# Optimization experiments

Hardware: AMD Instinct MI355X
Metric: run time of the kernel (lower is better)

The kernel has to match this reference:

```python
import jax, jax.numpy as jnp
import numpy as np
import math

N = 65536
IN_FEATURES = 64
OUT_FEATURES = 64
N_MODES = 32
N_BASIS = 1 + 2 * N_MODES


def setup_inputs() -> dict:
    key = jax.random.key(0)
    k1, k2 = jax.random.split(key)
    x = jax.random.normal(k1, (N, IN_FEATURES), dtype=jnp.float32)
    coeffs = jax.random.normal(k2, (OUT_FEATURES, IN_FEATURES, N_BASIS), dtype=jnp.float32) * 0.1
    bias = jnp.zeros((OUT_FEATURES,), dtype=jnp.float32)
    return {"x": x, "coeffs": coeffs, "bias": bias}


def reference(x, coeffs, bias):
    # freqs: [modes] = (1..modes) * pi
    freqs = jnp.arange(1, N_MODES + 1, dtype=x.dtype) * jnp.asarray(math.pi, dtype=x.dtype)
    x_flat = x.reshape(-1, IN_FEATURES)                      # [n, i]
    angles = x_flat[..., None] * freqs                       # [n, i, m]
    ones = jnp.ones(x_flat.shape + (1,), dtype=x.dtype)      # [n, i, 1]
    basis = jnp.concatenate([ones, jnp.sin(angles), jnp.cos(angles)], axis=-1)  # [n, i, b]
    out = jnp.einsum('oib,nib->no', coeffs, basis) + bias    # [n, o]
    return out.reshape(*x.shape[:-1], OUT_FEATURES)
```

## Files before the change

### kernel.cpp

```cpp
#include <hip/hip_runtime.h>
#include <hip/hip_bf16.h>


typedef __bf16 bf16x8 __attribute__((ext_vector_type(8)));
typedef float  f32x4  __attribute__((ext_vector_type(4)));
typedef float  f32x16 __attribute__((ext_vector_type(16)));

#define PI_F 3.14159265358979323846f

__global__ __launch_bounds__(256) void fkan_repack(
    const float* __restrict__ coeffs, __bf16* __restrict__ Bp,
    float* __restrict__ bias2sum) {
  int gid = blockIdx.x * 256 + threadIdx.x;
  if (gid >= 64 * 64 * 65) return;
  float v = coeffs[gid];
  int b  = gid % 65;
  int oi = gid / 65;
  int i = oi & 63;
  int o = oi >> 6;
  if (b == 0) {
    atomicAdd(&bias2sum[o], v);
    return;
  }
  int m  = (b - 1) & 31;
  int sc = (b >= 33) ? 1 : 0;
  int kc = i >> 3;
  int kq = (i >> 2) & 1;
  int cc = o >> 5;
  int frag = (m * 8 + kc) * 2 + cc;
  int lane = kq * 32 + (o & 31);
  int t = 2 * (i & 3) + sc;
  Bp[frag * 512 + lane * 8 + t] = (__bf16)v;
}

__device__ __forceinline__ void stage_slice(const __bf16* __restrict__ Bp,
                                            __bf16* dst, int m, int wave,
                                            int lane) {
  const char* g = (const char*)Bp + (size_t)m * 16384 + wave * 4096 + lane * 16;
  char* l = (char*)dst + wave * 4096;
  #pragma unroll
  for (int r = 0; r < 4; ++r) {
    __builtin_amdgcn_global_load_lds(
        (const __attribute__((address_space(1))) void*)(g + r * 1024),
        (__attribute__((address_space(3))) void*)(l + r * 1024), 16, 0, 0);
  }
}

__global__ __launch_bounds__(256, 1) void fkan_main(
    const float* __restrict__ x, const __bf16* __restrict__ Bp,
    const float* __restrict__ bias, const float* __restrict__ bias2sum,
    float* __restrict__ out) {
  __shared__ __bf16 Bs[2][8192];

  int tid  = threadIdx.x;
  int wave = tid >> 6;
  int lane = tid & 63;
  int kq   = lane >> 5;
  int cl   = lane & 31;
  int rowbase = blockIdx.x * 256 + wave * 64;

  float s1[64], c1[64], sm[64], cm[64];
  #pragma unroll
  for (int t = 0; t < 2; ++t) {
    const float* xrow = x + (size_t)(rowbase + t * 32 + cl) * 64 + kq * 4;
    #pragma unroll
    for (int kc = 0; kc < 8; ++kc) {
      f32x4 v = *(const f32x4*)(xrow + kc * 8);
      #pragma unroll
      for (int e = 0; e < 4; ++e) {
        int p = t * 32 + kc * 4 + e;
        float ss, cs;
        __sincosf(PI_F * v[e], &ss, &cs);
        s1[p] = ss; c1[p] = cs;
        sm[p] = ss; cm[p] = cs;
      }
    }
  }

  f32x16 acc[2][2];
  #pragma unroll
  for (int t = 0; t < 2; ++t)
    #pragma unroll
    for (int c2 = 0; c2 < 2; ++c2)
      #pragma unroll
      for (int r = 0; r < 16; ++r) acc[t][c2][r] = 0.f;

  stage_slice(Bp, &Bs[0][0], 0, wave, lane);
  __syncthreads();

  for (int m = 0; m < 32; ++m) {
    int buf = m & 1;
    if (m < 31) stage_slice(Bp, &Bs[buf ^ 1][0], m + 1, wave, lane);

    #pragma unroll
    for (int kc = 0; kc < 8; ++kc) {
      bf16x8 af0, af1;
      #pragma unroll
      for (int e = 0; e < 4; ++e) {
        af0[2 * e]     = (__bf16)sm[kc * 4 + e];
        af0[2 * e + 1] = (__bf16)cm[kc * 4 + e];
        af1[2 * e]     = (__bf16)sm[32 + kc * 4 + e];
        af1[2 * e + 1] = (__bf16)cm[32 + kc * 4 + e];
      }
      #pragma unroll
      for (int c2 = 0; c2 < 2; ++c2) {
        bf16x8 bf = *(const bf16x8*)(&Bs[buf][(kc * 2 + c2) * 512 + lane * 8]);
        acc[0][c2] = __builtin_amdgcn_mfma_f32_32x32x16_bf16(af0, bf,
                                                             acc[0][c2], 0, 0, 0);
        acc[1][c2] = __builtin_amdgcn_mfma_f32_32x32x16_bf16(af1, bf,
                                                             acc[1][c2], 0, 0, 0);
      }
    }

    if (m < 31) {
      #pragma unroll
      for (int p = 0; p < 64; ++p) {
        float t0 = sm[p];
        sm[p] = fmaf(t0, c1[p],  cm[p] * s1[p]);
        cm[p] = fmaf(cm[p], c1[p], -t0 * s1[p]);
      }
    }
    __syncthreads();
  }

  #pragma unroll
  for (int c2 = 0; c2 < 2; ++c2) {
    float bv = bias[c2 * 32 + cl] + bias2sum[c2 * 32 + cl];
    #pragma unroll
    for (int t = 0; t < 2; ++t) {
      float* orow = out + (size_t)(rowbase + t * 32) * 64;
      #pragma unroll
      for (int r = 0; r < 16; ++r) {
        int ro = (r & 3) + 8 * (r >> 2) + 4 * kq;
        orow[(size_t)ro * 64 + c2 * 32 + cl] = acc[t][c2][r] + bv;
      }
    }
  }
}

extern "C" void kernel_launch(void* const* d_in, const int* in_sizes, int n_in,
                              void* d_out, int out_size, void* d_ws, size_t ws_size,
                              hipStream_t stream) {
  const float* x      = (const float*)d_in[0];
  const float* coeffs = (const float*)d_in[1];
  const float* bias   = (const float*)d_in[2];
  float* out = (float*)d_out;

  __bf16* Bp      = (__bf16*)d_ws;
  float* bias2sum = (float*)((char*)d_ws + 512 * 1024);

  int n_rows = in_sizes[0] / 64;

  hipMemsetAsync(bias2sum, 0, 64 * sizeof(float), stream);
  fkan_repack<<<(64 * 64 * 65 + 255) / 256, 256, 0, stream>>>(coeffs, Bp,
                                                              bias2sum);
  fkan_main<<<n_rows / 256, 256, 0, stream>>>(x, Bp, bias, bias2sum, out);
}
```

Before: 140.1 us.

## Split work across waves by input half and column half, use Chebyshev recurrence

Each block now handles 64 rows, and its four waves split the reduction into two input-feature halves and the outputs into two column halves. This cuts per-thread register state (32 instead of 64 angle entries) and allows two blocks per CU with four times as many blocks. The angle-addition rotation is replaced by a three-term Chebyshev recurrence that takes one FMA per value and processes two modes per iteration, staging B in pairs. The two input halves are added through LDS at the end, which costs an extra sync and LDS round trip, and the recurrence may lose precision differently from the rotation.

```diff
diff --git a/kernel.cpp b/kernel.cpp
--- a/kernel.cpp
+++ b/kernel.cpp
@@ -33,106 +33,133 @@
   Bp[frag * 512 + lane * 8 + t] = (__bf16)v;
 }
 
-__device__ __forceinline__ void stage_slice(const __bf16* __restrict__ Bp,
-                                            __bf16* dst, int m, int wave,
-                                            int lane) {
-  const char* g = (const char*)Bp + (size_t)m * 16384 + wave * 4096 + lane * 16;
-  char* l = (char*)dst + wave * 4096;
+__device__ __forceinline__ void stage_pair(const __bf16* __restrict__ Bp,
+                                           __bf16* dst, int pair, int wave,
+                                           int lane) {
+  const char* g = (const char*)Bp + (size_t)pair * 32768 + wave * 1024 + lane * 16;
+  char* l = (char*)dst + wave * 1024;
   #pragma unroll
-  for (int r = 0; r < 4; ++r) {
+  for (int r = 0; r < 8; ++r) {
     __builtin_amdgcn_global_load_lds(
-        (const __attribute__((address_space(1))) void*)(g + r * 1024),
-        (__attribute__((address_space(3))) void*)(l + r * 1024), 16, 0, 0);
+        (const __attribute__((address_space(1))) void*)(g + r * 4096),
+        (__attribute__((address_space(3))) void*)(l + r * 4096), 16, 0, 0);
   }
 }
 
-__global__ __launch_bounds__(256, 1) void fkan_main(
+__global__ __launch_bounds__(256, 2) void fkan_main(
     const float* __restrict__ x, const __bf16* __restrict__ Bp,
     const float* __restrict__ bias, const float* __restrict__ bias2sum,
     float* __restrict__ out) {
-  __shared__ __bf16 Bs[2][8192];
+  __shared__ __bf16 Bs[2][16384];
 
   int tid  = threadIdx.x;
   int wave = tid >> 6;
   int lane = tid & 63;
   int kq   = lane >> 5;
   int cl   = lane & 31;
-  int rowbase = blockIdx.x * 256 + wave * 64;
+  int ih   = wave >> 1;
+  int cw   = wave & 1;
+  int rowbase = blockIdx.x * 64;
 
-  float s1[64], c1[64], sm[64], cm[64];
+  float sC[32], cC[32], sP[32], cP[32], Tch[32];
   #pragma unroll
   for (int t = 0; t < 2; ++t) {
-    const float* xrow = x + (size_t)(rowbase + t * 32 + cl) * 64 + kq * 4;
+    const float* xrow =
+        x + (size_t)(rowbase + t * 32 + cl) * 64 + ih * 32 + kq * 4;
     #pragma unroll
-    for (int kc = 0; kc < 8; ++kc) {
+    for (int kc = 0; kc < 4; ++kc) {
       f32x4 v = *(const f32x4*)(xrow + kc * 8);
       #pragma unroll
       for (int e = 0; e < 4; ++e) {
-        int p = t * 32 + kc * 4 + e;
+        int p = t * 16 + kc * 4 + e;
         float ss, cs;
         __sincosf(PI_F * v[e], &ss, &cs);
-        s1[p] = ss; c1[p] = cs;
-        sm[p] = ss; cm[p] = cs;
+        sC[p] = ss;  cC[p] = cs;
+        sP[p] = 0.f; cP[p] = 1.f;
+        Tch[p] = 2.0f * cs;
       }
     }
   }
 
-  f32x16 acc[2][2];
+  f32x16 acc[2];
   #pragma unroll
   for (int t = 0; t < 2; ++t)
     #pragma unroll
-    for (int c2 = 0; c2 < 2; ++c2)
-      #pragma unroll
-      for (int r = 0; r < 16; ++r) acc[t][c2][r] = 0.f;
+    for (int r = 0; r < 16; ++r) acc[t][r] = 0.f;
 
-  stage_slice(Bp, &Bs[0][0], 0, wave, lane);
+  stage_pair(Bp, &Bs[0][0], 0, wave, lane);
   __syncthreads();
 
-  for (int m = 0; m < 32; ++m) {
-    int buf = m & 1;
-    if (m < 31) stage_slice(Bp, &Bs[buf ^ 1][0], m + 1, wave, lane);
+  for (int p = 0; p < 16; ++p) {
+    int buf = p & 1;
+    if (p < 15) stage_pair(Bp, &Bs[buf ^ 1][0], p + 1, wave, lane);
 
     #pragma unroll
-    for (int kc = 0; kc < 8; ++kc) {
-      bf16x8 af0, af1;
+    for (int kc = 0; kc < 4; ++kc) {
+      bf16x8 bfr = *(const bf16x8*)(
+          &Bs[buf][((ih * 4 + kc) * 2 + cw) * 512 + lane * 8]);
       #pragma unroll
-      for (int e = 0; e < 4; ++e) {
-        af0[2 * e]     = (__bf16)sm[kc * 4 + e];
-        af0[2 * e + 1] = (__bf16)cm[kc * 4 + e];
-        af1[2 * e]     = (__bf16)sm[32 + kc * 4 + e];
-        af1[2 * e + 1] = (__bf16)cm[32 + kc * 4 + e];
-      }
-      #pragma unroll
-      for (int c2 = 0; c2 < 2; ++c2) {
-        bf16x8 bf = *(const bf16x8*)(&Bs[buf][(kc * 2 + c2) * 512 + lane * 8]);
-        acc[0][c2] = __builtin_amdgcn_mfma_f32_32x32x16_bf16(af0, bf,
-                                                             acc[0][c2], 0, 0, 0);
-        acc[1][c2] = __builtin_amdgcn_mfma_f32_32x32x16_bf16(af1, bf,
-                                                             acc[1][c2], 0, 0, 0);
+      for (int t = 0; t < 2; ++t) {
+        bf16x8 af;
+        #pragma unroll
+        for (int e = 0; e < 4; ++e) {
+          af[2 * e]     = (__bf16)sC[t * 16 + kc * 4 + e];
+          af[2 * e + 1] = (__bf16)cC[t * 16 + kc * 4 + e];
+        }
+        acc[t] = __builtin_amdgcn_mfma_f32_32x32x16_bf16(af, bfr, acc[t],
+                                                         0, 0, 0);
       }
     }
+    #pragma unroll
+    for (int q = 0; q < 32; ++q) {
+      sP[q] = fmaf(Tch[q], sC[q], -sP[q]);
+      cP[q] = fmaf(Tch[q], cC[q], -cP[q]);
+    }
 
-    if (m < 31) {
+    #pragma unroll
+    for (int kc = 0; kc < 4; ++kc) {
+      bf16x8 bfr = *(const bf16x8*)(
+          &Bs[buf][8192 + ((ih * 4 + kc) * 2 + cw) * 512 + lane * 8]);
       #pragma unroll
-      for (int p = 0; p < 64; ++p) {
-        float t0 = sm[p];
-        sm[p] = fmaf(t0, c1[p],  cm[p] * s1[p]);
-        cm[p] = fmaf(cm[p], c1[p], -t0 * s1[p]);
+      for (int t = 0; t < 2; ++t) {
+        bf16x8 af;
+        #pragma unroll
+        for (int e = 0; e < 4; ++e) {
+          af[2 * e]     = (__bf16)sP[t * 16 + kc * 4 + e];
+          af[2 * e + 1] = (__bf16)cP[t * 16 + kc * 4 + e];
+        }
+        acc[t] = __builtin_amdgcn_mfma_f32_32x32x16_bf16(af, bfr, acc[t],
+                                                         0, 0, 0);
       }
+    }
+    #pragma unroll
+    for (int q = 0; q < 32; ++q) {
+      sC[q] = fmaf(Tch[q], sP[q], -sC[q]);
+      cC[q] = fmaf(Tch[q], cP[q], -cC[q]);
     }
     __syncthreads();
   }
 
-  #pragma unroll
-  for (int c2 = 0; c2 < 2; ++c2) {
-    float bv = bias[c2 * 32 + cl] + bias2sum[c2 * 32 + cl];
+  float* Lf = (float*)&Bs[0][0];
+  if (ih == 1) {
+    #pragma unroll
+    for (int t = 0; t < 2; ++t)
+      #pragma unroll
+      for (int r = 0; r < 16; ++r)
+        Lf[cw * 2048 + t * 1024 + r * 64 + lane] = acc[t][r];
+  }
+  __syncthreads();
+  if (ih == 0) {
+    int col = cw * 32 + cl;
+    float bv = bias[col] + bias2sum[col];
     #pragma unroll
     for (int t = 0; t < 2; ++t) {
       float* orow = out + (size_t)(rowbase + t * 32) * 64;
       #pragma unroll
       for (int r = 0; r < 16; ++r) {
+        float sum = acc[t][r] + Lf[cw * 2048 + t * 1024 + r * 64 + lane];
         int ro = (r & 3) + 8 * (r >> 2) + 4 * kq;
-        orow[(size_t)ro * 64 + c2 * 32 + cl] = acc[t][c2][r] + bv;
+        orow[(size_t)ro * 64 + col] = sum + bv;
       }
     }
   }
@@ -154,5 +181,5 @@
   hipMemsetAsync(bias2sum, 0, 64 * sizeof(float), stream);
   fkan_repack<<<(64 * 64 * 65 + 255) / 256, 256, 0, stream>>>(coeffs, Bp,
                                                               bias2sum);
-  fkan_main<<<n_rows / 256, 256, 0, stream>>>(x, Bp, bias, bias2sum, out);
+  fkan_main<<<n_rows / 64, 256, 0, stream>>>(x, Bp, bias, bias2sum, out);
 }
```

Result: no change. 141.2 us (+0.8%).
